# Kernel optimization log

Hardware: AMD Instinct MI355X
Metric: run time of the kernel (lower is better)

Reference implementation:

```python
import jax, jax.numpy as jnp
import numpy as np

BS, DOP, RAN, AZI, ELE = 2, 32, 128, 128, 32
INTERVAL = 0.1
TAU = 1.0


def setup_inputs() -> dict:
    key = jax.random.key(0)
    ks = jax.random.split(key, 7)
    N = RAN * AZI * ELE
    seg = jax.random.normal(ks[0], (BS, N, 1), jnp.float32)
    flow = jax.random.normal(ks[1], (BS, N, 3), jnp.float32) * 2.0
    x1 = jax.random.normal(ks[2], (BS, DOP, RAN, AZI, ELE), jnp.float32)
    dop_arr = jax.random.normal(ks[3], (BS, DOP), jnp.float32)
    coords = jax.random.uniform(ks[4], (BS, 3, RAN, AZI, ELE), jnp.float32)
    ori = jax.random.normal(ks[5], (BS, 3, RAN, AZI, ELE), jnp.float32)
    u = jax.random.uniform(ks[6], (BS, DOP, RAN, AZI, ELE), jnp.float32,
                           minval=1e-6, maxval=1.0 - 1e-6)
    gumbels = -jnp.log(-jnp.log(u))  # Gumbel(0,1) noise (sampled internally in torch)
    return {"seg": seg, "flow": flow, "x1": x1, "dop_arr": dop_arr,
            "coords": coords, "ori": ori, "gumbels": gumbels}


def _gather3d(vol_flat, z, y, x, H, W):
    # vol_flat: (B, C, D*H*W); z,y,x: (B, D, H, W) int32
    B = vol_flat.shape[0]
    idx = ((z * H + y) * W + x).reshape(B, 1, -1)
    g = jnp.take_along_axis(vol_flat, idx, axis=2)
    return g  # (B, C, N)


def _grid_sample_3d_border(vol, gx, gy, gz):
    # Trilinear grid_sample, padding_mode='border', align_corners=True.
    # vol: (B, C, D, H, W); gx/gy/gz: (B, D, H, W) normalized coords in [-1, 1]
    B, C, D, H, W = vol.shape
    ix = jnp.clip((gx + 1.0) * 0.5 * (W - 1), 0.0, W - 1.0)
    iy = jnp.clip((gy + 1.0) * 0.5 * (H - 1), 0.0, H - 1.0)
    iz = jnp.clip((gz + 1.0) * 0.5 * (D - 1), 0.0, D - 1.0)
    x0f, y0f, z0f = jnp.floor(ix), jnp.floor(iy), jnp.floor(iz)
    wx, wy, wz = ix - x0f, iy - y0f, iz - z0f
    x0 = jnp.clip(x0f.astype(jnp.int32), 0, W - 1)
    y0 = jnp.clip(y0f.astype(jnp.int32), 0, H - 1)
    z0 = jnp.clip(z0f.astype(jnp.int32), 0, D - 1)
    x1 = jnp.clip(x0 + 1, 0, W - 1)
    y1 = jnp.clip(y0 + 1, 0, H - 1)
    z1 = jnp.clip(z0 + 1, 0, D - 1)
    vf = vol.reshape(B, C, -1)
    out = jnp.zeros((B, C, D * H * W), vol.dtype)
    for zc, wzc in ((z0, 1.0 - wz), (z1, wz)):
        for yc, wyc in ((y0, 1.0 - wy), (y1, wy)):
            for xc, wxc in ((x0, 1.0 - wx), (x1, wx)):
                w = (wzc * wyc * wxc).reshape(B, 1, -1)
                out = out + w * _gather3d(vf, zc, yc, xc, H, W)
    return out.reshape(B, C, D, H, W)


def _warp_flowxyz(coords, flo):
    B, C, D, H, W = coords.shape
    zz = jnp.arange(D, dtype=jnp.float32)[:, None, None]
    yy = jnp.arange(H, dtype=jnp.float32)[None, :, None]
    xx = jnp.arange(W, dtype=jnp.float32)[None, None, :]
    # vgrid = base grid + flow, per channel (x, y, z)
    vx = xx + flo[:, 0]
    vy = yy + flo[:, 1]
    vz = zz + flo[:, 2]
    gx = 2.0 * vx / (W - 1) - 1.0
    gy = 2.0 * vy / (H - 1) - 1.0
    gz = 2.0 * vz / (D - 1) - 1.0
    r, a, e = coords[:, 0], coords[:, 1], coords[:, 2]
    ce = jnp.cos(e)
    xyz = jnp.stack([r * ce * jnp.cos(a), r * ce * jnp.sin(a), r * jnp.sin(e)], axis=1)
    xyz_new = _grid_sample_3d_border(xyz, gx, gy, gz)
    return xyz_new - xyz


def reference(seg, flow, x1, dop_arr, coords, ori, gumbels):
    bs, dop, ran, azi, ele = x1.shape
    dop_b = dop_arr.reshape(bs, dop, 1, 1, 1)
    # gumbel_softmax(hard=True): forward value is the hard one-hot
    y_soft = jax.nn.softmax((x1 + gumbels) / TAU, axis=1)
    idx = jnp.argmax(y_soft, axis=1)
    y_hard = jax.nn.one_hot(idx, dop, axis=1, dtype=x1.dtype)
    max_x1 = y_hard + y_soft - jax.lax.stop_gradient(y_soft)  # straight-through
    softmax_x1 = jax.nn.softmax(x1, axis=1)
    x1_dop1 = jnp.sum(max_x1 * dop_b, axis=1, keepdims=True)
    x1_dop2 = jnp.sum(softmax_x1 * dop_b, axis=1, keepdims=True)
    x1_dop = jnp.concatenate([x1_dop1, x1_dop2], axis=1)  # (bs, 2, R, A, E)
    seg_v = jnp.transpose(seg, (0, 2, 1)).reshape(bs, -1, ran, azi, ele)
    flow_v = jnp.transpose(flow, (0, 2, 1)).reshape(bs, -1, ran, azi, ele)
    flow_xyz = _warp_flowxyz(coords, flow_v)
    velo = flow_xyz / INTERVAL
    dop_label = jnp.sum(velo * ori, axis=1, keepdims=True)
    dop_error = (dop_label - x1_dop) ** 2
    seg_label = jax.nn.sigmoid(10.0 * (0.15 - dop_error))
    seg_label = jnp.mean(seg_label, axis=1, keepdims=True)
    seg_sig = jax.nn.sigmoid(seg_v)
    loss = jnp.mean(jnp.abs(seg_sig - seg_label))
    return loss
```

## Files before the change

kernel.cpp:

```cpp
#include <hip/hip_runtime.h>
#include <math.h>

#define BSZ  2
#define DOPN 32
#define RAN  128
#define AZI  128
#define ELE  32
#define NVOX (RAN * AZI * ELE)
#define TPB  256
#define VPT  2
#define DH   16

__device__ __forceinline__ float sigmoidf_(float t) {
    return 1.0f / (1.0f + __expf(-t));
}

__global__ __launch_bounds__(TPB) void xyz_precompute(
    const float* __restrict__ coords, float4* __restrict__ xyz4)
{
    const int n = blockIdx.x * TPB + threadIdx.x;
    const int b = blockIdx.y;
    const float* cb = coords + (size_t)b * 3 * NVOX;
    const float r = cb[n];
    const float a = cb[NVOX + n];
    const float e = cb[2 * NVOX + n];
    float sa, ca, se, ce;
    __sincosf(a, &sa, &ca);
    __sincosf(e, &se, &ce);
    xyz4[(size_t)b * NVOX + n] = make_float4(r * ce * ca, r * ce * sa, r * se, 0.0f);
}

__global__ __launch_bounds__(TPB) void seg_dop_loss(
    const float* __restrict__ seg, const float* __restrict__ flow,
    const float* __restrict__ x1, const float* __restrict__ dop_arr,
    const float* __restrict__ ori, const float* __restrict__ gumbels,
    const float4* __restrict__ xyz4, float* __restrict__ out)
{
    __shared__ float s_dop[DOPN];
    __shared__ float s_wave[TPB / 64];

    const int b = blockIdx.y;
    if (threadIdx.x < DOPN) s_dop[threadIdx.x] = dop_arr[b * DOPN + threadIdx.x];
    __syncthreads();

    const int n0 = (blockIdx.x * TPB + threadIdx.x) * VPT;
    const size_t base = (size_t)b * DOPN * NVOX + (size_t)n0;

    float m_lg[VPT] = { -3.4e38f, -3.4e38f };
    float ssum[VPT] = { 0.f, 0.f };
    float wsum[VPT] = { 0.f, 0.f };
    int   idx[VPT]  = { 0, 0 };

    for (int h = 0; h < 2; ++h) {
        const size_t dbase = base + (size_t)h * DH * NVOX;
        float2 xa[DH], ga[DH];
        #pragma unroll
        for (int d = 0; d < DH; ++d)
            xa[d] = *(const float2*)(x1 + dbase + (size_t)d * NVOX);
        #pragma unroll
        for (int d = 0; d < DH; ++d)
            ga[d] = *(const float2*)(gumbels + dbase + (size_t)d * NVOX);
        #pragma unroll
        for (int d = 0; d < DH; ++d) {
            const int dg = h * DH + d;
            const float dv = s_dop[dg];
            const float xv[VPT] = { xa[d].x, xa[d].y };
            const float gv[VPT] = { ga[d].x, ga[d].y };
            #pragma unroll
            for (int v = 0; v < VPT; ++v) {
                const float lg = xv[v] + gv[v];
                if (lg > m_lg[v]) { m_lg[v] = lg; idx[v] = dg; }
                const float ev = __expf(xv[v]);
                ssum[v] += ev;
                wsum[v] += ev * dv;
            }
        }
    }

    const float* fl = flow + ((size_t)b * NVOX + (size_t)n0) * 3;
    float fbuf[3 * VPT];
    *(float2*)(fbuf)     = *(const float2*)(fl);
    *(float2*)(fbuf + 2) = *(const float2*)(fl + 2);
    *(float2*)(fbuf + 4) = *(const float2*)(fl + 4);

    const float4* xb4 = xyz4 + (size_t)b * NVOX;
    float4 bxyz[VPT];
    #pragma unroll
    for (int v = 0; v < VPT; ++v) bxyz[v] = xb4[n0 + v];

    const float* ob = ori + (size_t)b * 3 * NVOX;
    const float2 oX2 = *(const float2*)(ob + n0);
    const float2 oY2 = *(const float2*)(ob + NVOX + n0);
    const float2 oZ2 = *(const float2*)(ob + 2 * NVOX + n0);
    const float oX[VPT] = { oX2.x, oX2.y };
    const float oY[VPT] = { oY2.x, oY2.y };
    const float oZ[VPT] = { oZ2.x, oZ2.y };

    const float2 sg2 = *(const float2*)(seg + (size_t)b * NVOX + n0);
    const float sg[VPT] = { sg2.x, sg2.y };

    const int xB = n0 & (ELE - 1);
    const int yI = (n0 >> 5) & (AZI - 1);
    const int zI = n0 >> 12;

    float contrib = 0.0f;
    #pragma unroll
    for (int v = 0; v < VPT; ++v) {
        const float vx = (float)(xB + v) + fbuf[3 * v + 0];
        const float vy = (float)yI       + fbuf[3 * v + 1];
        const float vz = (float)zI       + fbuf[3 * v + 2];

        const float gx = 2.0f * vx / (float)(ELE - 1) - 1.0f;
        const float gy = 2.0f * vy / (float)(AZI - 1) - 1.0f;
        const float gz = 2.0f * vz / (float)(RAN - 1) - 1.0f;
        const float ix = fminf(fmaxf((gx + 1.0f) * 0.5f * (float)(ELE - 1), 0.0f), (float)(ELE - 1));
        const float iy = fminf(fmaxf((gy + 1.0f) * 0.5f * (float)(AZI - 1), 0.0f), (float)(AZI - 1));
        const float iz = fminf(fmaxf((gz + 1.0f) * 0.5f * (float)(RAN - 1), 0.0f), (float)(RAN - 1));

        const float x0f = floorf(ix), y0f = floorf(iy), z0f = floorf(iz);
        const float wx = ix - x0f, wy = iy - y0f, wz = iz - z0f;
        int x0 = (int)x0f; x0 = x0 < 0 ? 0 : (x0 > ELE - 1 ? ELE - 1 : x0);
        int y0 = (int)y0f; y0 = y0 < 0 ? 0 : (y0 > AZI - 1 ? AZI - 1 : y0);
        int z0 = (int)z0f; z0 = z0 < 0 ? 0 : (z0 > RAN - 1 ? RAN - 1 : z0);
        const int x1c = x0 + 1 > ELE - 1 ? ELE - 1 : x0 + 1;
        const int y1c = y0 + 1 > AZI - 1 ? AZI - 1 : y0 + 1;
        const int z1c = z0 + 1 > RAN - 1 ? RAN - 1 : z0 + 1;

        const int m00 = (z0  * AZI + y0 ) * ELE;
        const int m01 = (z0  * AZI + y1c) * ELE;
        const int m10 = (z1c * AZI + y0 ) * ELE;
        const int m11 = (z1c * AZI + y1c) * ELE;
        const float4 c000 = xb4[m00 + x0],  c001 = xb4[m00 + x1c];
        const float4 c010 = xb4[m01 + x0],  c011 = xb4[m01 + x1c];
        const float4 c100 = xb4[m10 + x0],  c101 = xb4[m10 + x1c];
        const float4 c110 = xb4[m11 + x0],  c111 = xb4[m11 + x1c];

        const float w000 = (1.0f - wz) * (1.0f - wy) * (1.0f - wx);
        const float w001 = (1.0f - wz) * (1.0f - wy) * wx;
        const float w010 = (1.0f - wz) * wy * (1.0f - wx);
        const float w011 = (1.0f - wz) * wy * wx;
        const float w100 = wz * (1.0f - wy) * (1.0f - wx);
        const float w101 = wz * (1.0f - wy) * wx;
        const float w110 = wz * wy * (1.0f - wx);
        const float w111 = wz * wy * wx;

        const float sX = w000*c000.x + w001*c001.x + w010*c010.x + w011*c011.x
                       + w100*c100.x + w101*c101.x + w110*c110.x + w111*c111.x;
        const float sY = w000*c000.y + w001*c001.y + w010*c010.y + w011*c011.y
                       + w100*c100.y + w101*c101.y + w110*c110.y + w111*c111.y;
        const float sZ = w000*c000.z + w001*c001.z + w010*c010.z + w011*c011.z
                       + w100*c100.z + w101*c101.z + w110*c110.z + w111*c111.z;

        const float vX = (sX - bxyz[v].x) * 10.0f;
        const float vY = (sY - bxyz[v].y) * 10.0f;
        const float vZ = (sZ - bxyz[v].z) * 10.0f;
        const float dop_label = vX * oX[v] + vY * oY[v] + vZ * oZ[v];

        const float dop1 = s_dop[idx[v]];
        const float dop2 = wsum[v] / ssum[v];
        float e1 = dop_label - dop1; e1 *= e1;
        float e2 = dop_label - dop2; e2 *= e2;
        const float seg_label = 0.5f * (sigmoidf_(10.0f * (0.15f - e1)) +
                                        sigmoidf_(10.0f * (0.15f - e2)));
        contrib += fabsf(sigmoidf_(sg[v]) - seg_label);
    }

    #pragma unroll
    for (int off = 32; off > 0; off >>= 1)
        contrib += __shfl_down(contrib, off, 64);
    const int lane = threadIdx.x & 63;
    const int wid  = threadIdx.x >> 6;
    if (lane == 0) s_wave[wid] = contrib;
    __syncthreads();
    if (threadIdx.x == 0) {
        float bsum = 0.0f;
        #pragma unroll
        for (int w = 0; w < TPB / 64; ++w) bsum += s_wave[w];
        atomicAdd(out, bsum * (1.0f / ((float)BSZ * (float)NVOX)));
    }
}

extern "C" void kernel_launch(void* const* d_in, const int* in_sizes, int n_in,
                              void* d_out, int out_size, void* d_ws, size_t ws_size,
                              hipStream_t stream) {
    const float* seg    = (const float*)d_in[0];
    const float* flow   = (const float*)d_in[1];
    const float* x1     = (const float*)d_in[2];
    const float* dopar  = (const float*)d_in[3];
    const float* coords = (const float*)d_in[4];
    const float* ori    = (const float*)d_in[5];
    const float* gumb   = (const float*)d_in[6];
    float* out = (float*)d_out;
    float4* xyz4 = (float4*)d_ws;

    hipMemsetAsync(d_out, 0, sizeof(float) * (size_t)out_size, stream);

    dim3 gridA(NVOX / TPB, BSZ);
    xyz_precompute<<<gridA, TPB, 0, stream>>>(coords, xyz4);
    dim3 gridB(NVOX / (TPB * VPT), BSZ);
    seg_dop_loss<<<gridB, TPB, 0, stream>>>(seg, flow, x1, dopar, ori, gumb, xyz4, out);
}
```

Baseline: 322.3 us.

## Double-buffer doppler channel loads and vectorize xyz precompute

The doppler-channel loop is split into four chunks of 8 with two register buffers, so loads for the next chunk are issued before the current chunk is consumed. The argmax now tracks the winning doppler value directly instead of an index, which avoids a dynamic shared-memory lookup. The xyz precompute kernel processes four voxels per thread with float4 loads and launches a quarter as many blocks. Register pressure stays similar, but the software pipelining depends on the compiler keeping the intended load order.

```diff
diff --git a/kernel.cpp b/kernel.cpp
--- a/kernel.cpp
+++ b/kernel.cpp
@@ -9,7 +9,7 @@
 #define NVOX (RAN * AZI * ELE)
 #define TPB  256
 #define VPT  2
-#define DH   16
+#define DH   8
 
 __device__ __forceinline__ float sigmoidf_(float t) {
     return 1.0f / (1.0f + __expf(-t));
@@ -18,16 +18,23 @@
 __global__ __launch_bounds__(TPB) void xyz_precompute(
     const float* __restrict__ coords, float4* __restrict__ xyz4)
 {
-    const int n = blockIdx.x * TPB + threadIdx.x;
+    const int n0 = (blockIdx.x * TPB + threadIdx.x) * 4;
     const int b = blockIdx.y;
     const float* cb = coords + (size_t)b * 3 * NVOX;
-    const float r = cb[n];
-    const float a = cb[NVOX + n];
-    const float e = cb[2 * NVOX + n];
-    float sa, ca, se, ce;
-    __sincosf(a, &sa, &ca);
-    __sincosf(e, &se, &ce);
-    xyz4[(size_t)b * NVOX + n] = make_float4(r * ce * ca, r * ce * sa, r * se, 0.0f);
+    const float4 r4 = *(const float4*)(cb + n0);
+    const float4 a4 = *(const float4*)(cb + NVOX + n0);
+    const float4 e4 = *(const float4*)(cb + 2 * NVOX + n0);
+    const float rr[4] = { r4.x, r4.y, r4.z, r4.w };
+    const float aa[4] = { a4.x, a4.y, a4.z, a4.w };
+    const float ee[4] = { e4.x, e4.y, e4.z, e4.w };
+    float4* op = xyz4 + (size_t)b * NVOX + n0;
+    #pragma unroll
+    for (int v = 0; v < 4; ++v) {
+        float sa, ca, se, ce;
+        __sincosf(aa[v], &sa, &ca);
+        __sincosf(ee[v], &se, &ce);
+        op[v] = make_float4(rr[v] * ce * ca, rr[v] * ce * sa, rr[v] * se, 0.0f);
+    }
 }
 
 __global__ __launch_bounds__(TPB) void seg_dop_loss(
@@ -47,35 +54,47 @@
     const size_t base = (size_t)b * DOPN * NVOX + (size_t)n0;
 
     float m_lg[VPT] = { -3.4e38f, -3.4e38f };
+    float mdop[VPT] = { 0.f, 0.f };
     float ssum[VPT] = { 0.f, 0.f };
     float wsum[VPT] = { 0.f, 0.f };
-    int   idx[VPT]  = { 0, 0 };
-
-    for (int h = 0; h < 2; ++h) {
-        const size_t dbase = base + (size_t)h * DH * NVOX;
-        float2 xa[DH], ga[DH];
-        #pragma unroll
-        for (int d = 0; d < DH; ++d)
-            xa[d] = *(const float2*)(x1 + dbase + (size_t)d * NVOX);
-        #pragma unroll
-        for (int d = 0; d < DH; ++d)
-            ga[d] = *(const float2*)(gumbels + dbase + (size_t)d * NVOX);
-        #pragma unroll
-        for (int d = 0; d < DH; ++d) {
-            const int dg = h * DH + d;
-            const float dv = s_dop[dg];
-            const float xv[VPT] = { xa[d].x, xa[d].y };
-            const float gv[VPT] = { ga[d].x, ga[d].y };
-            #pragma unroll
-            for (int v = 0; v < VPT; ++v) {
-                const float lg = xv[v] + gv[v];
-                if (lg > m_lg[v]) { m_lg[v] = lg; idx[v] = dg; }
-                const float ev = __expf(xv[v]);
-                ssum[v] += ev;
-                wsum[v] += ev * dv;
-            }
+
+    float2 Ax[DH], Ag[DH], Bx[DH], Bg[DH];
+
+    #define LOADC(BX, BG, H)                                                   \
+        _Pragma("unroll")                                                      \
+        for (int d = 0; d < DH; ++d) {                                         \
+            const size_t p = base + (size_t)((H) * DH + d) * NVOX;             \
+            BX[d] = *(const float2*)(x1 + p);                                  \
+            BG[d] = *(const float2*)(gumbels + p);                             \
         }
-    }
+
+    #define CONSC(BX, BG, H)                                                   \
+        _Pragma("unroll")                                                      \
+        for (int d = 0; d < DH; ++d) {                                         \
+            const float dv = s_dop[(H) * DH + d];                              \
+            const float xv[VPT] = { BX[d].x, BX[d].y };                        \
+            const float gv[VPT] = { BG[d].x, BG[d].y };                        \
+            _Pragma("unroll")                                                  \
+            for (int v = 0; v < VPT; ++v) {                                    \
+                const float lg = xv[v] + gv[v];                 \
+                if (lg > m_lg[v]) { m_lg[v] = lg; mdop[v] = dv; }              \
+                const float ev = __expf(xv[v]);                                \
+                ssum[v] += ev;                                                 \
+                wsum[v] += ev * dv;                                            \
+            }                                                                  \
+        }
+
+    LOADC(Ax, Ag, 0);
+    LOADC(Bx, Bg, 1);
+    CONSC(Ax, Ag, 0);
+    LOADC(Ax, Ag, 2);
+    CONSC(Bx, Bg, 1);
+    LOADC(Bx, Bg, 3);
+    CONSC(Ax, Ag, 2);
+    CONSC(Bx, Bg, 3);
+
+    #undef LOADC
+    #undef CONSC
 
     const float* fl = flow + ((size_t)b * NVOX + (size_t)n0) * 3;
     float fbuf[3 * VPT];
@@ -156,7 +175,7 @@
         const float vZ = (sZ - bxyz[v].z) * 10.0f;
         const float dop_label = vX * oX[v] + vY * oY[v] + vZ * oZ[v];
 
-        const float dop1 = s_dop[idx[v]];
+        const float dop1 = mdop[v];
         const float dop2 = wsum[v] / ssum[v];
         float e1 = dop_label - dop1; e1 *= e1;
         float e2 = dop_label - dop2; e2 *= e2;
@@ -195,7 +214,7 @@
 
     hipMemsetAsync(d_out, 0, sizeof(float) * (size_t)out_size, stream);
 
-    dim3 gridA(NVOX / TPB, BSZ);
+    dim3 gridA(NVOX / (TPB * 4), BSZ);
     xyz_precompute<<<gridA, TPB, 0, stream>>>(coords, xyz4);
     dim3 gridB(NVOX / (TPB * VPT), BSZ);
     seg_dop_loss<<<gridB, TPB, 0, stream>>>(seg, flow, x1, dopar, ori, gumb, xyz4, out);
```

After: 327.1 us. Within noise of the previous version (+1.5%).
